# Kernel tuning notes

Measured on AMD Instinct MI355X. Metric: run time of the kernel, lower is better.

## Reference

```python
import jax, jax.numpy as jnp
import numpy as np

NEG_SLOPE = 0.01  # torch F.leaky_relu default
EPS = 1e-12


def setup_inputs() -> dict:
    key = jax.random.key(0)
    k1, k2, k3, k4 = jax.random.split(key, 4)
    num_nodes, in_f, out_f, num_edges = 50000, 128, 128, 600000
    x = jax.random.normal(k1, (num_nodes, in_f), dtype=jnp.float32)
    edge_index = jax.random.randint(k2, (2, num_edges), 0, num_nodes, dtype=jnp.int64)
    # xavier_uniform for W:[out,in]
    limit = float(np.sqrt(6.0 / (in_f + out_f)))
    W = jax.random.uniform(k3, (out_f, in_f), dtype=jnp.float32, minval=-limit, maxval=limit)
    a = jax.random.uniform(k4, (2 * out_f,), dtype=jnp.float32, minval=0.0, maxval=1.0)
    return {"x": x, "edge_index": edge_index, "W": W, "a": a}


def reference(x, edge_index, W, a):
    num_nodes = x.shape[0]
    out_f = W.shape[0]
    # add self loops
    loops = jnp.arange(num_nodes, dtype=edge_index.dtype)
    src = jnp.concatenate([edge_index[0], loops])
    dst = jnp.concatenate([edge_index[1], loops])
    messages = x @ W.T                      # [N, F_out]
    # cat([h_src,h_dst]) @ a == h_src @ a[:F] + h_dst @ a[F:] (avoids materializing concat)
    s_src = messages @ a[:out_f]            # [N]
    s_dst = messages @ a[out_f:]            # [N]
    e_ij = jax.nn.leaky_relu(s_src[src] + s_dst[dst], negative_slope=NEG_SLOPE)  # [E]
    w = jnp.exp(e_ij)                       # unnormalized edge weights
    denom = jax.ops.segment_sum(w, dst, num_segments=num_nodes)
    denom = jnp.maximum(denom, EPS)
    weighted = w[:, None] * messages[src]   # [E, F_out]
    agg = jax.ops.segment_sum(weighted, dst, num_segments=num_nodes)
    return agg / denom[:, None]
```

## Files before the change

### kernel.cpp

```cpp
#include <hip/hip_runtime.h>

#define NEG_SLOPE 0.01f
#define CAP 64

typedef __attribute__((ext_vector_type(8))) short bf16x8;
typedef __attribute__((ext_vector_type(4))) float f32x4;

static __device__ __forceinline__ unsigned short f2bf(float f) {
  unsigned u = __float_as_uint(f);
  u += 0x7fffu + ((u >> 16) & 1u);
  return (unsigned short)(u >> 16);
}

__global__ __launch_bounds__(256) void k_setup(const float* __restrict__ W,
                                               const float* __restrict__ a,
                                               unsigned short* __restrict__ Wb,
                                               float* __restrict__ p_lo,
                                               float* __restrict__ p_hi,
                                               int* __restrict__ counts, int N, int nz) {
  int b = blockIdx.x;
  int t = threadIdx.x;
  if (b < nz) {
    int i = b * 256 + t;
    if (i < N) counts[i] = 0;
  } else if (b < nz + 64) {
    int i = (b - nz) * 256 + t;
    Wb[i] = f2bf(W[i]);
  } else {
    if (t < 128) {
      float lo = 0.f, hi = 0.f;
#pragma unroll 8
      for (int f = 0; f < 128; ++f) {
        float w = W[f * 128 + t];
        lo += w * a[f];
        hi += w * a[128 + f];
      }
      p_lo[t] = lo;
      p_hi[t] = hi;
    }
  }
}

__global__ __launch_bounds__(256) void k_msg(const float* __restrict__ x,
                                             const float* __restrict__ p_lo,
                                             const float* __restrict__ p_hi,
                                             const unsigned short* __restrict__ Wb,
                                             unsigned short* __restrict__ msgs,
                                             float* __restrict__ s_src,
                                             float* __restrict__ s_dst, int N) {
  int wave = (blockIdx.x * 256 + threadIdx.x) >> 6;
  int lane = threadIdx.x & 63;
  int base = wave * 16;
  if (base >= N) return;
  int q = lane >> 4, r = lane & 15;
  int node = base + r;
  const float* xrow = x + (size_t)node * 128 + q * 8;
  const float4* pl = (const float4*)p_lo;
  const float4* ph = (const float4*)p_hi;
  bf16x8 afrag[4];
  float lo = 0.f, hi = 0.f;
#pragma unroll
  for (int c = 0; c < 4; ++c) {
    float4 v0 = *(const float4*)(xrow + c * 32);
    float4 v1 = *(const float4*)(xrow + c * 32 + 4);
    int fi = q * 2 + c * 8;
    float4 a0 = pl[fi], a1 = pl[fi + 1];
    float4 b0 = ph[fi], b1 = ph[fi + 1];
    lo += v0.x * a0.x + v0.y * a0.y + v0.z * a0.z + v0.w * a0.w
        + v1.x * a1.x + v1.y * a1.y + v1.z * a1.z + v1.w * a1.w;
    hi += v0.x * b0.x + v0.y * b0.y + v0.z * b0.z + v0.w * b0.w
        + v1.x * b1.x + v1.y * b1.y + v1.z * b1.z + v1.w * b1.w;
    bf16x8 f;
    f[0] = (short)f2bf(v0.x); f[1] = (short)f2bf(v0.y);
    f[2] = (short)f2bf(v0.z); f[3] = (short)f2bf(v0.w);
    f[4] = (short)f2bf(v1.x); f[5] = (short)f2bf(v1.y);
    f[6] = (short)f2bf(v1.z); f[7] = (short)f2bf(v1.w);
    afrag[c] = f;
  }
  lo += __shfl_xor(lo, 16); lo += __shfl_xor(lo, 32);
  hi += __shfl_xor(hi, 16); hi += __shfl_xor(hi, 32);
  if (q == 0) { s_src[node] = lo; s_dst[node] = hi; }
#pragma unroll
  for (int ft = 0; ft < 8; ++ft) {
    const unsigned short* wrow = Wb + (size_t)(ft * 16 + r) * 128 + q * 8;
    f32x4 acc = {0.f, 0.f, 0.f, 0.f};
#pragma unroll
    for (int c = 0; c < 4; ++c) {
      bf16x8 bfrag = *(const bf16x8*)(wrow + c * 32);
      acc = __builtin_amdgcn_mfma_f32_16x16x32_bf16(afrag[c], bfrag, acc, 0, 0, 0);
    }
#pragma unroll
    for (int rr = 0; rr < 4; ++rr) {
      int n2 = base + q * 4 + rr;
      msgs[(size_t)n2 * 128 + ft * 16 + r] = f2bf(acc[rr]);
    }
  }
}

__global__ __launch_bounds__(256) void k_scatter(const int* __restrict__ ei,
                                                 int* __restrict__ counts,
                                                 unsigned* __restrict__ edges, int E) {
  int e2 = blockIdx.x * 256 + threadIdx.x;
  int e = e2 * 2;
  if (e >= E) return;
  int s0 = __builtin_nontemporal_load(ei + e);
  int s1 = __builtin_nontemporal_load(ei + e + 1);
  int d0 = __builtin_nontemporal_load(ei + E + e);
  int d1 = __builtin_nontemporal_load(ei + E + e + 1);
  int pos0 = atomicAdd(&counts[d0], 1);
  if (pos0 < CAP)
    __builtin_nontemporal_store((unsigned)s0, edges + (size_t)d0 * CAP + pos0);
  if (e + 1 < E) {
    int pos1 = atomicAdd(&counts[d1], 1);
    if (pos1 < CAP)
      __builtin_nontemporal_store((unsigned)s1, edges + (size_t)d1 * CAP + pos1);
  }
}

__global__ __launch_bounds__(256) void k_agg(const unsigned short* __restrict__ msgs,
                                             const int* __restrict__ counts,
                                             const unsigned* __restrict__ edges,
                                             const float* __restrict__ s_src,
                                             const float* __restrict__ s_dst,
                                             float* __restrict__ out, int N) {
  int wave = (blockIdx.x * 256 + threadIdx.x) >> 6;
  int lane = threadIdx.x & 63;
  if (wave >= N) return;
  int node = wave;
  int g = lane >> 4;
  int r = lane & 15;
  float sdn = s_dst[node];
  float zs = s_src[node] + sdn;
  zs = zs > 0.f ? zs : NEG_SLOPE * zs;
  float wself = expf(zs);
  float wg = (g == 0) ? wself : 0.f;
  float denom = wg;
  float acc[8];
  {
    const uint4* mrow = (const uint4*)(msgs + (size_t)node * 128);
    uint4 m = mrow[r];
    unsigned mm[4] = {m.x, m.y, m.z, m.w};
#pragma unroll
    for (int c = 0; c < 4; ++c) {
      acc[2 * c]     = wg * __uint_as_float(mm[c] << 16);
      acc[2 * c + 1] = wg * __uint_as_float(mm[c] & 0xffff0000u);
    }
  }
  int cnt = counts[node];
  cnt = cnt < CAP ? cnt : CAP;
  const unsigned* bucket = edges + (size_t)node * CAP;
  int nIter = (cnt + 15) >> 4;
  for (int it = 0; it < nIter; ++it) {
    int kb = it * 16 + g;
    bool v[4];
    unsigned e[4];
    uint4 m[4];
    float ss[4];
#pragma unroll
    for (int u = 0; u < 4; ++u) {
      int k = kb + u * 4;
      v[u] = k < cnt;
      e[u] = bucket[v[u] ? k : 0];
    }
#pragma unroll
    for (int u = 0; u < 4; ++u)
      m[u] = ((const uint4*)(msgs + (size_t)e[u] * 128))[r];
#pragma unroll
    for (int u = 0; u < 4; ++u)
      ss[u] = s_src[e[u]];
#pragma unroll
    for (int u = 0; u < 4; ++u) {
      float z = ss[u] + sdn;
      z = z > 0.f ? z : NEG_SLOPE * z;
      float w = v[u] ? expf(z) : 0.f;
      unsigned mm[4] = {m[u].x, m[u].y, m[u].z, m[u].w};
#pragma unroll
      for (int c = 0; c < 4; ++c) {
        acc[2 * c]     += w * __uint_as_float(mm[c] << 16);
        acc[2 * c + 1] += w * __uint_as_float(mm[c] & 0xffff0000u);
      }
      denom += w;
    }
  }
#pragma unroll
  for (int mask = 16; mask < 64; mask <<= 1) {
#pragma unroll
    for (int j = 0; j < 8; ++j) acc[j] += __shfl_xor(acc[j], mask);
    denom += __shfl_xor(denom, mask);
  }
  if (g == 0) {
    float inv = 1.f / fmaxf(denom, 1e-12f);
    float4 o0 = {acc[0] * inv, acc[1] * inv, acc[2] * inv, acc[3] * inv};
    float4 o1 = {acc[4] * inv, acc[5] * inv, acc[6] * inv, acc[7] * inv};
    float4* orow = (float4*)(out + (size_t)node * 128);
    orow[r * 2] = o0;
    orow[r * 2 + 1] = o1;
  }
}

extern "C" void kernel_launch(void* const* d_in, const int* in_sizes, int n_in,
                              void* d_out, int out_size, void* d_ws, size_t ws_size,
                              hipStream_t stream) {
  const float* x = (const float*)d_in[0];
  const int* ei = (const int*)d_in[1];
  const float* W = (const float*)d_in[2];
  const float* a = (const float*)d_in[3];
  float* out = (float*)d_out;
  int N = in_sizes[0] / 128;
  int E = in_sizes[1] / 2;

  char* ws = (char*)d_ws;
  size_t off = 0;
  auto alloc = [&](size_t bytes) {
    off = (off + 255) & ~(size_t)255;
    void* p = ws + off;
    off += bytes;
    return p;
  };
  unsigned short* msgs = (unsigned short*)alloc((size_t)N * 128 * 2);
  float* s_src = (float*)alloc((size_t)N * 4);
  float* s_dst = (float*)alloc((size_t)N * 4);
  float* p_lo = (float*)alloc(512);
  float* p_hi = (float*)alloc(512);
  unsigned short* Wb = (unsigned short*)alloc(128 * 128 * 2);
  int* counts = (int*)alloc((size_t)N * 4);
  unsigned* edges = (unsigned*)alloc((size_t)N * CAP * 4);

  int nz = (N + 255) / 256;
  int waves = (N + 15) / 16;
  k_setup<<<nz + 64 + 1, 256, 0, stream>>>(W, a, Wb, p_lo, p_hi, counts, N, nz);
  k_scatter<<<((E + 1) / 2 + 255) / 256, 256, 0, stream>>>(ei, counts, edges, E);
  k_msg<<<(waves + 3) / 4, 256, 0, stream>>>(x, p_lo, p_hi, Wb, msgs, s_src, s_dst, N);
  k_agg<<<(N + 3) / 4, 256, 0, stream>>>(msgs, counts, edges, s_src, s_dst, out, N);
}
```

Before: 168.7 us.

## Fuse edge scatter and message GEMM into one kernel launch

Merges the independent edge-bucketing scatter kernel and the MFMA message/score kernel into a single launch, with block index ranges selecting the role. This removes one launch and lets the atomic-bound scatter blocks run alongside the compute-bound GEMM blocks instead of serialising. It also swaps the nontemporal scalar loads and stores for plain int2 vector loads and ordinary stores, which changes the cache behaviour of the edge buffer writes. Register use of the fused kernel is set by the larger GEMM path, which may lower occupancy for the scatter blocks.

```diff
diff --git a/kernel.cpp b/kernel.cpp
--- a/kernel.cpp
+++ b/kernel.cpp
@@ -41,14 +41,33 @@
   }
 }
 
-__global__ __launch_bounds__(256) void k_msg(const float* __restrict__ x,
-                                             const float* __restrict__ p_lo,
-                                             const float* __restrict__ p_hi,
-                                             const unsigned short* __restrict__ Wb,
-                                             unsigned short* __restrict__ msgs,
-                                             float* __restrict__ s_src,
-                                             float* __restrict__ s_dst, int N) {
-  int wave = (blockIdx.x * 256 + threadIdx.x) >> 6;
+__global__ __launch_bounds__(256) void k_work(const float* __restrict__ x,
+                                              const float* __restrict__ p_lo,
+                                              const float* __restrict__ p_hi,
+                                              const unsigned short* __restrict__ Wb,
+                                              unsigned short* __restrict__ msgs,
+                                              float* __restrict__ s_src,
+                                              float* __restrict__ s_dst, int N,
+                                              const int* __restrict__ ei,
+                                              int* __restrict__ counts,
+                                              unsigned* __restrict__ edges, int E,
+                                              int SB) {
+  if ((int)blockIdx.x < SB) {
+    int e2 = blockIdx.x * 256 + threadIdx.x;
+    int e = e2 * 2;
+    if (e >= E) return;
+    int2 srcp = *(const int2*)(ei + e);
+    int2 dstp = *(const int2*)(ei + E + e);
+    int pos0 = atomicAdd(&counts[dstp.x], 1);
+    if (pos0 < CAP) edges[(size_t)dstp.x * CAP + pos0] = (unsigned)srcp.x;
+    if (e + 1 < E) {
+      int pos1 = atomicAdd(&counts[dstp.y], 1);
+      if (pos1 < CAP) edges[(size_t)dstp.y * CAP + pos1] = (unsigned)srcp.y;
+    }
+    return;
+  }
+  int bb = blockIdx.x - SB;
+  int wave = (bb * 256 + (int)threadIdx.x) >> 6;
   int lane = threadIdx.x & 63;
   int base = wave * 16;
   if (base >= N) return;
@@ -94,26 +113,6 @@
       int n2 = base + q * 4 + rr;
       msgs[(size_t)n2 * 128 + ft * 16 + r] = f2bf(acc[rr]);
     }
-  }
-}
-
-__global__ __launch_bounds__(256) void k_scatter(const int* __restrict__ ei,
-                                                 int* __restrict__ counts,
-                                                 unsigned* __restrict__ edges, int E) {
-  int e2 = blockIdx.x * 256 + threadIdx.x;
-  int e = e2 * 2;
-  if (e >= E) return;
-  int s0 = __builtin_nontemporal_load(ei + e);
-  int s1 = __builtin_nontemporal_load(ei + e + 1);
-  int d0 = __builtin_nontemporal_load(ei + E + e);
-  int d1 = __builtin_nontemporal_load(ei + E + e + 1);
-  int pos0 = atomicAdd(&counts[d0], 1);
-  if (pos0 < CAP)
-    __builtin_nontemporal_store((unsigned)s0, edges + (size_t)d0 * CAP + pos0);
-  if (e + 1 < E) {
-    int pos1 = atomicAdd(&counts[d1], 1);
-    if (pos1 < CAP)
-      __builtin_nontemporal_store((unsigned)s1, edges + (size_t)d1 * CAP + pos1);
   }
 }
 
@@ -228,8 +227,10 @@
 
   int nz = (N + 255) / 256;
   int waves = (N + 15) / 16;
+  int SB = ((E + 1) / 2 + 255) / 256;
+  int MB = (waves + 3) / 4;
   k_setup<<<nz + 64 + 1, 256, 0, stream>>>(W, a, Wb, p_lo, p_hi, counts, N, nz);
-  k_scatter<<<((E + 1) / 2 + 255) / 256, 256, 0, stream>>>(ei, counts, edges, E);
-  k_msg<<<(waves + 3) / 4, 256, 0, stream>>>(x, p_lo, p_hi, Wb, msgs, s_src, s_dst, N);
+  k_work<<<SB + MB, 256, 0, stream>>>(x, p_lo, p_hi, Wb, msgs, s_src, s_dst, N,
+                                      ei, counts, edges, E, SB);
   k_agg<<<(N + 3) / 4, 256, 0, stream>>>(msgs, counts, edges, s_src, s_dst, out, N);
 }
```

Measured after the change: 159.5 us. 5.4% less time.
